# Kernel optimization log

Hardware: AMD Instinct MI355X
Metric: run time of the kernel (lower is better)

The kernel has to match this reference:

```python
import jax, jax.numpy as jnp
import numpy as np

INVALID = 1e9  # distance value marking a missing arc (>= 1e6 threshold in source)
TEMPERATURE = 0.5


def setup_inputs() -> dict:
    n = 4096
    key = jax.random.key(0)
    k_d, k_m, k_l = jax.random.split(key, 3)
    dist = jax.random.uniform(k_d, (n, n), dtype=jnp.float32, minval=0.0, maxval=100.0)
    keep = jax.random.uniform(k_m, (n, n)) < 0.5
    distance_matrix = jnp.where(keep, dist, INVALID).astype(jnp.float32)
    logits = (-2.0 + 0.5 * jax.random.normal(k_l, (n, n))).astype(jnp.float32)
    attention_logits = jnp.zeros((n, n), dtype=jnp.float32)
    return {
        "distance_matrix": distance_matrix,
        "logits": logits,
        "attention_logits": attention_logits,
        "source": 0,
        "destination": n - 1,
    }


def reference(distance_matrix, logits, attention_logits, source, destination):
    n = distance_matrix.shape[0]
    valid = (distance_matrix < 1e6).astype(jnp.float32)
    density = jnp.sum(valid) / (n * n)
    mu1 = 1.0
    mu2 = 10.0 * (1.0 + density)
    mu3 = 10.0 * (1.0 + density)

    # decision matrix (dense branch)
    attention = jax.nn.softmax(attention_logits, axis=1)
    x = jax.nn.sigmoid(logits / TEMPERATURE) * attention * valid  # [n, n]

    # flow penalty: vectorized form of the per-node loop
    out_flow = jnp.sum(x, axis=1)  # [n]
    in_flow = jnp.sum(x, axis=0)   # [n]
    d = out_flow - in_flow
    d = d.at[source].add(-1.0).at[destination].add(1.0)
    flow_penalty = jnp.sum(d * d)

    path_cost = jnp.sum(distance_matrix * x)  # invalid arcs have x == 0
    binary_penalty = jnp.sum(x * (1.0 - x))

    # connectivity: 10-step matmul power iteration (min(n-1, 10) = 10 for n > 11)
    reach = x
    for _ in range(10):
        reach = jnp.minimum(reach + reach @ x, 1.0)
    connectivity_penalty = jnp.square(1.0 - reach[source, destination])

    sparsity_penalty = jnp.sum(x) / (n * n)
    n_edges = jnp.sum(valid)

    return (mu1 * path_cost / (n_edges + 1e-6)
            + mu2 * flow_penalty / n
            + mu3 * binary_penalty / (n * n)
            + 20.0 * connectivity_penalty
            + 5.0 * sparsity_penalty)
```

## Files before the change

### kernel.cpp

```cpp
#include <hip/hip_runtime.h>
#include <hip/hip_bf16.h>
#include <cmath>

typedef unsigned short u16;
typedef unsigned int u32;

__device__ __forceinline__ float bf2f(u16 b) {
    return __uint_as_float(((u32)b) << 16);
}
__device__ __forceinline__ u16 f2bf(float f) {
    u32 u = __float_as_uint(f);
    u = (u + 0x7fffu + ((u >> 16) & 1u)) >> 16;
    return (u16)u;
}

__device__ __forceinline__ float wave_sum(float v) {
#pragma unroll
    for (int o = 32; o > 0; o >>= 1) v += __shfl_xor(v, o, 64);
    return v;
}

__device__ float block_sum(float v) {
    __shared__ float s[4];
    v = wave_sum(v);
    __syncthreads();
    if ((threadIdx.x & 63) == 0) s[threadIdx.x >> 6] = v;
    __syncthreads();
    return s[0] + s[1] + s[2] + s[3];
}

template <int K>
__global__ __launch_bounds__(256, 4) void k_x(
    const float* __restrict__ dist, const float* __restrict__ logit,
    const float* __restrict__ attn, const int* __restrict__ srcp,
    u16* __restrict__ xb, float* __restrict__ out_flow,
    float* __restrict__ cnt_row, float* __restrict__ s2_row,
    float* __restrict__ pc_row, float* __restrict__ v, int n) {
    const int row = blockIdx.x;
    const int t = threadIdx.x;
    const size_t base = (size_t)row * n;

    float4 a4[K];
#pragma unroll
    for (int k = 0; k < K; ++k)
        a4[k] = *(const float4*)(attn + base + 4 * t + 1024 * k);
    float se = 0.f;
#pragma unroll
    for (int k = 0; k < K; ++k) {
        a4[k].x = __expf(a4[k].x); a4[k].y = __expf(a4[k].y);
        a4[k].z = __expf(a4[k].z); a4[k].w = __expf(a4[k].w);
        se += (a4[k].x + a4[k].y) + (a4[k].z + a4[k].w);
    }
    const float invZ = 1.0f / block_sum(se);
    const int src = *srcp;

    float4 d4[K], l4[K];
#pragma unroll
    for (int k = 0; k < K; ++k) {
        const int col = 4 * t + 1024 * k;
        d4[k] = *(const float4*)(dist + base + col);
        l4[k] = *(const float4*)(logit + base + col);
    }
    float cnt = 0.f, s1 = 0.f, s2 = 0.f, pc = 0.f;
#pragma unroll
    for (int k = 0; k < K; ++k) {
        const int col = 4 * t + 1024 * k;
        const float av[4] = {a4[k].x, a4[k].y, a4[k].z, a4[k].w};
        const float dv[4] = {d4[k].x, d4[k].y, d4[k].z, d4[k].w};
        const float lv[4] = {l4[k].x, l4[k].y, l4[k].z, l4[k].w};
        float xv[4];
        ushort4 pk;
        u16* pkp = (u16*)&pk;
#pragma unroll
        for (int q = 0; q < 4; ++q) {
            float valid = (dv[q] < 1.0e6f) ? 1.f : 0.f;
            float sg = 1.0f / (1.0f + __expf(-2.0f * lv[q]));
            float x = sg * (av[q] * invZ) * valid;
            xv[q] = x;
            cnt += valid;
            s1 += x;
            s2 += x * x;
            pc += dv[q] * x;
            pkp[q] = f2bf(x);
        }
        *(ushort4*)(xb + base + col) = pk;
        if (row == src) {
            float4 vf; vf.x = xv[0]; vf.y = xv[1]; vf.z = xv[2]; vf.w = xv[3];
            *(float4*)(v + col) = vf;
        }
    }
    s1 = block_sum(s1);
    cnt = block_sum(cnt);
    s2 = block_sum(s2);
    pc = block_sum(pc);
    if (t == 0) {
        out_flow[row] = s1;
        cnt_row[row] = cnt;
        s2_row[row] = s2;
        pc_row[row] = pc;
    }
}

template <int FIRST>
__global__ __launch_bounds__(256) void k_iter(
    const u16* __restrict__ xb, const float* __restrict__ v_in,
    const float* __restrict__ up_in, float* __restrict__ v_out,
    float* __restrict__ up_out, float* __restrict__ ip,
    int n, int nbx, int rc) {
    __shared__ float vl[64];
    __shared__ float vparts[4][64];
    const int t = threadIdx.x;
    const int lin = blockIdx.x;
    const int xcd = lin & 7;
    const int slot = lin >> 3;
    const int bx = slot % nbx;
    const int by = xcd * ((gridDim.x >> 3) / nbx) + slot / nbx;
    const int rows_per = n / rc;
    const int i0 = by * rows_per;
    const int j0 = bx * 1024 + t * 4;

    if (FIRST) {
        if (t < rows_per) {
            float a = v_in[i0 + t];
            vl[t] = a;
            if (bx == 0) v_out[i0 + t] = a;
        }
    } else {
        const int i = t & 63, g = t >> 6;
        const int cpg = rc >> 2;
        float a = 0.f;
#pragma unroll 4
        for (int c = g * cpg; c < (g + 1) * cpg; ++c)
            a += up_in[(size_t)c * n + i0 + i];
        vparts[g][i] = a;
        __syncthreads();
        if (t < rows_per) {
            float s = v_in[i0 + t] + vparts[0][t] + vparts[1][t] +
                      vparts[2][t] + vparts[3][t];
            vl[t] = s;
            if (bx == 0) v_out[i0 + t] = s;
        }
    }
    __syncthreads();

    float4 acc = {0.f, 0.f, 0.f, 0.f};
    float4 cs = {0.f, 0.f, 0.f, 0.f};
#pragma unroll 8
    for (int i = 0; i < rows_per; ++i) {
        ushort4 xv = *(const ushort4*)(xb + (size_t)(i0 + i) * n + j0);
        float vi = vl[i];
        acc.x = fmaf(vi, bf2f(xv.x), acc.x);
        acc.y = fmaf(vi, bf2f(xv.y), acc.y);
        acc.z = fmaf(vi, bf2f(xv.z), acc.z);
        acc.w = fmaf(vi, bf2f(xv.w), acc.w);
        if (FIRST) {
            cs.x += bf2f(xv.x); cs.y += bf2f(xv.y);
            cs.z += bf2f(xv.z); cs.w += bf2f(xv.w);
        }
    }
    *(float4*)(up_out + (size_t)by * n + j0) = acc;
    if (FIRST) *(float4*)(ip + (size_t)by * n + j0) = cs;
}

__global__ __launch_bounds__(256) void k_reduce(
    const float* __restrict__ out_flow, const float* __restrict__ ip,
    const float* __restrict__ cnt_row, const float* __restrict__ s2_row,
    const float* __restrict__ pc_row, const int* __restrict__ srcp,
    const int* __restrict__ dstp, float* __restrict__ pb, int n, int nchunk) {
    const int t = threadIdx.x;
    const int j = blockIdx.x * 256 + t;
    const int src = *srcp, dst = *dstp;
    float infl = 0.f;
#pragma unroll 8
    for (int c = 0; c < nchunk; ++c) infl += ip[(size_t)c * n + j];
    float d = out_flow[j] - infl;
    if (j == src) d -= 1.f;
    if (j == dst) d += 1.f;
    float f = block_sum(d * d);
    float s1 = block_sum(out_flow[j]);
    float cnt = block_sum(cnt_row[j]);
    float s2 = block_sum(s2_row[j]);
    float pc = block_sum(pc_row[j]);
    if (t == 0) {
        float* p = pb + blockIdx.x * 5;
        p[0] = f; p[1] = s1; p[2] = cnt; p[3] = s2; p[4] = pc;
    }
}

__global__ __launch_bounds__(256) void k_final(
    const float* __restrict__ pb, const float* __restrict__ v_last,
    const float* __restrict__ up_last, const int* __restrict__ dstp,
    float* __restrict__ out, int n, int nblk, int nchunk) {
    const int t = threadIdx.x;
    const int dst = *dstp;
    float flow = block_sum(t < nblk ? pb[t * 5 + 0] : 0.f);
    float S1   = block_sum(t < nblk ? pb[t * 5 + 1] : 0.f);
    float NE   = block_sum(t < nblk ? pb[t * 5 + 2] : 0.f);
    float S2   = block_sum(t < nblk ? pb[t * 5 + 3] : 0.f);
    float PC   = block_sum(t < nblk ? pb[t * 5 + 4] : 0.f);
    float r = block_sum(t < nchunk ? up_last[(size_t)t * n + dst] : 0.f);
    if (t == 0) {
        r += v_last[dst];
        float nf = (float)n;
        float nn = nf * nf;
        float density = NE / nn;
        float mu2 = 10.f * (1.f + density);
        float om = 1.f - r;
        float res = PC / (NE + 1e-6f)
                  + mu2 * flow / nf
                  + mu2 * (S1 - S2) / nn
                  + 20.f * om * om
                  + 5.f * S1 / nn;
        out[0] = res;
    }
}

extern "C" void kernel_launch(void* const* d_in, const int* in_sizes, int n_in,
                              void* d_out, int out_size, void* d_ws, size_t ws_size,
                              hipStream_t stream) {
    const float* dist = (const float*)d_in[0];
    const float* logit = (const float*)d_in[1];
    const float* attn = (const float*)d_in[2];
    const int* srcp = (const int*)d_in[3];
    const int* dstp = (const int*)d_in[4];
    const int n = (int)(std::sqrt((double)in_sizes[0]) + 0.5);
    const size_t nn = (size_t)n * n;

    const int RC = 64;
    const int nbx = n / 1024;

    char* ws = (char*)d_ws;
    u16* xb = (u16*)ws;
    float* f = (float*)(ws + nn * sizeof(u16));
    float* out_flow = f; f += n;
    float* cnt_row = f;  f += n;
    float* s2_row = f;   f += n;
    float* pc_row = f;   f += n;
    float* vA = f;       f += n;
    float* vB = f;       f += n;
    float* upA = f;      f += (size_t)RC * n;
    float* upB = f;      f += (size_t)RC * n;
    float* ip = f;       f += (size_t)RC * n;
    float* pb = f;       f += 128;

    switch (n >> 10) {
        case 4: k_x<4><<<n, 256, 0, stream>>>(dist, logit, attn, srcp, xb,
                    out_flow, cnt_row, s2_row, pc_row, vA, n); break;
        case 2: k_x<2><<<n, 256, 0, stream>>>(dist, logit, attn, srcp, xb,
                    out_flow, cnt_row, s2_row, pc_row, vA, n); break;
        case 8: k_x<8><<<n, 256, 0, stream>>>(dist, logit, attn, srcp, xb,
                    out_flow, cnt_row, s2_row, pc_row, vA, n); break;
        default: k_x<1><<<n, 256, 0, stream>>>(dist, logit, attn, srcp, xb,
                    out_flow, cnt_row, s2_row, pc_row, vA, n); break;
    }

    const int niblk = nbx * RC;

    k_iter<1><<<niblk, 256, 0, stream>>>(xb, vA, nullptr, vB, upA, ip, n, nbx, RC);
    float* vin = vB;  float* uin = upA;
    float* vout;      float* uout;
    for (int it = 2; it <= 10; ++it) {
        vout = (it & 1) ? vB : vA;
        uout = (it & 1) ? upA : upB;
        k_iter<0><<<niblk, 256, 0, stream>>>(xb, vin, uin, vout, uout, nullptr,
                                             n, nbx, RC);
        vin = vout; uin = uout;
    }

    k_reduce<<<n / 256, 256, 0, stream>>>(out_flow, ip, cnt_row, s2_row,
                                          pc_row, srcp, dstp, pb, n, RC);
    k_final<<<1, 256, 0, stream>>>(pb, vin, uin, dstp, (float*)d_out, n,
                                   n / 256, RC);
}
```

Before: 113.1 us.

## Defer softmax normalisation to per-row scale factors applied downstream

The x kernel no longer does a block reduction for the softmax denominator before computing x. It stores unnormalised values, accumulates all row sums in a single pass, and writes a per-row inverse normaliser. The power-iteration and column-sum kernels then fold that row scale into the vector weights. The aim is to remove a sync point and register pressure in k_x (the occupancy hint is also dropped). In exchange, the stored bf16 matrix is unnormalised, which changes rounding, and a few extra per-row loads are added in k_iter.

```diff
diff --git a/kernel.cpp b/kernel.cpp
--- a/kernel.cpp
+++ b/kernel.cpp
@@ -30,74 +30,62 @@
 }
 
 template <int K>
-__global__ __launch_bounds__(256, 4) void k_x(
+__global__ __launch_bounds__(256) void k_x(
     const float* __restrict__ dist, const float* __restrict__ logit,
     const float* __restrict__ attn, const int* __restrict__ srcp,
     u16* __restrict__ xb, float* __restrict__ out_flow,
     float* __restrict__ cnt_row, float* __restrict__ s2_row,
-    float* __restrict__ pc_row, float* __restrict__ v, int n) {
+    float* __restrict__ pc_row, float* __restrict__ v,
+    float* __restrict__ izrow, int n) {
     const int row = blockIdx.x;
     const int t = threadIdx.x;
     const size_t base = (size_t)row * n;
-
-    float4 a4[K];
-#pragma unroll
-    for (int k = 0; k < K; ++k)
-        a4[k] = *(const float4*)(attn + base + 4 * t + 1024 * k);
-    float se = 0.f;
-#pragma unroll
-    for (int k = 0; k < K; ++k) {
-        a4[k].x = __expf(a4[k].x); a4[k].y = __expf(a4[k].y);
-        a4[k].z = __expf(a4[k].z); a4[k].w = __expf(a4[k].w);
-        se += (a4[k].x + a4[k].y) + (a4[k].z + a4[k].w);
-    }
-    const float invZ = 1.0f / block_sum(se);
     const int src = *srcp;
-
-    float4 d4[K], l4[K];
-#pragma unroll
+    float se = 0.f, cnt = 0.f, s1 = 0.f, s2 = 0.f, pc = 0.f;
+#pragma unroll 2
     for (int k = 0; k < K; ++k) {
         const int col = 4 * t + 1024 * k;
-        d4[k] = *(const float4*)(dist + base + col);
-        l4[k] = *(const float4*)(logit + base + col);
-    }
-    float cnt = 0.f, s1 = 0.f, s2 = 0.f, pc = 0.f;
-#pragma unroll
-    for (int k = 0; k < K; ++k) {
-        const int col = 4 * t + 1024 * k;
-        const float av[4] = {a4[k].x, a4[k].y, a4[k].z, a4[k].w};
-        const float dv[4] = {d4[k].x, d4[k].y, d4[k].z, d4[k].w};
-        const float lv[4] = {l4[k].x, l4[k].y, l4[k].z, l4[k].w};
-        float xv[4];
+        const float4 af = *(const float4*)(attn + base + col);
+        const float4 df = *(const float4*)(dist + base + col);
+        const float4 lf = *(const float4*)(logit + base + col);
+        const float ev[4] = {__expf(af.x), __expf(af.y),
+                             __expf(af.z), __expf(af.w)};
+        const float dv[4] = {df.x, df.y, df.z, df.w};
+        const float lv[4] = {lf.x, lf.y, lf.z, lf.w};
+        float yv[4];
         ushort4 pk;
         u16* pkp = (u16*)&pk;
 #pragma unroll
         for (int q = 0; q < 4; ++q) {
             float valid = (dv[q] < 1.0e6f) ? 1.f : 0.f;
             float sg = 1.0f / (1.0f + __expf(-2.0f * lv[q]));
-            float x = sg * (av[q] * invZ) * valid;
-            xv[q] = x;
+            float y = sg * ev[q] * valid;
+            yv[q] = y;
+            se += ev[q];
             cnt += valid;
-            s1 += x;
-            s2 += x * x;
-            pc += dv[q] * x;
-            pkp[q] = f2bf(x);
+            s1 += y;
+            s2 += y * y;
+            pc += dv[q] * y;
+            pkp[q] = f2bf(y);
         }
         *(ushort4*)(xb + base + col) = pk;
         if (row == src) {
-            float4 vf; vf.x = xv[0]; vf.y = xv[1]; vf.z = xv[2]; vf.w = xv[3];
-            *(float4*)(v + col) = vf;
-        }
-    }
+            float4 vf; vf.x = yv[0]; vf.y = yv[1]; vf.z = yv[2]; vf.w = yv[3];
+            *(float4*)(v + base ? v + col : v + col) = vf;
+        }
+    }
+    se = block_sum(se);
     s1 = block_sum(s1);
     cnt = block_sum(cnt);
     s2 = block_sum(s2);
     pc = block_sum(pc);
     if (t == 0) {
-        out_flow[row] = s1;
+        const float iz = 1.0f / se;
+        izrow[row] = iz;
+        out_flow[row] = s1 * iz;
         cnt_row[row] = cnt;
-        s2_row[row] = s2;
-        pc_row[row] = pc;
+        s2_row[row] = s2 * iz * iz;
+        pc_row[row] = pc * iz;
     }
 }
 
@@ -106,8 +94,10 @@
     const u16* __restrict__ xb, const float* __restrict__ v_in,
     const float* __restrict__ up_in, float* __restrict__ v_out,
     float* __restrict__ up_out, float* __restrict__ ip,
+    const float* __restrict__ izrow, const int* __restrict__ srcp,
     int n, int nbx, int rc) {
     __shared__ float vl[64];
+    __shared__ float wz[64];
     __shared__ float vparts[4][64];
     const int t = threadIdx.x;
     const int lin = blockIdx.x;
@@ -121,8 +111,11 @@
 
     if (FIRST) {
         if (t < rows_per) {
-            float a = v_in[i0 + t];
-            vl[t] = a;
+            const float iz_src = izrow[*srcp];
+            const float a = v_in[i0 + t] * iz_src;
+            const float iz = izrow[i0 + t];
+            vl[t] = a * iz;
+            wz[t] = iz;
             if (bx == 0) v_out[i0 + t] = a;
         }
     } else {
@@ -135,9 +128,9 @@
         vparts[g][i] = a;
         __syncthreads();
         if (t < rows_per) {
-            float s = v_in[i0 + t] + vparts[0][t] + vparts[1][t] +
-                      vparts[2][t] + vparts[3][t];
-            vl[t] = s;
+            const float s = v_in[i0 + t] + vparts[0][t] + vparts[1][t] +
+                            vparts[2][t] + vparts[3][t];
+            vl[t] = s * izrow[i0 + t];
             if (bx == 0) v_out[i0 + t] = s;
         }
     }
@@ -154,8 +147,11 @@
         acc.z = fmaf(vi, bf2f(xv.z), acc.z);
         acc.w = fmaf(vi, bf2f(xv.w), acc.w);
         if (FIRST) {
-            cs.x += bf2f(xv.x); cs.y += bf2f(xv.y);
-            cs.z += bf2f(xv.z); cs.w += bf2f(xv.w);
+            float wi = wz[i];
+            cs.x = fmaf(wi, bf2f(xv.x), cs.x);
+            cs.y = fmaf(wi, bf2f(xv.y), cs.y);
+            cs.z = fmaf(wi, bf2f(xv.z), cs.z);
+            cs.w = fmaf(wi, bf2f(xv.w), cs.w);
         }
     }
     *(float4*)(up_out + (size_t)by * n + j0) = acc;
@@ -238,6 +234,7 @@
     float* pc_row = f;   f += n;
     float* vA = f;       f += n;
     float* vB = f;       f += n;
+    float* izrow = f;    f += n;
     float* upA = f;      f += (size_t)RC * n;
     float* upB = f;      f += (size_t)RC * n;
     float* ip = f;       f += (size_t)RC * n;
@@ -245,25 +242,26 @@
 
     switch (n >> 10) {
         case 4: k_x<4><<<n, 256, 0, stream>>>(dist, logit, attn, srcp, xb,
-                    out_flow, cnt_row, s2_row, pc_row, vA, n); break;
+                    out_flow, cnt_row, s2_row, pc_row, vA, izrow, n); break;
         case 2: k_x<2><<<n, 256, 0, stream>>>(dist, logit, attn, srcp, xb,
-                    out_flow, cnt_row, s2_row, pc_row, vA, n); break;
+                    out_flow, cnt_row, s2_row, pc_row, vA, izrow, n); break;
         case 8: k_x<8><<<n, 256, 0, stream>>>(dist, logit, attn, srcp, xb,
-                    out_flow, cnt_row, s2_row, pc_row, vA, n); break;
+                    out_flow, cnt_row, s2_row, pc_row, vA, izrow, n); break;
         default: k_x<1><<<n, 256, 0, stream>>>(dist, logit, attn, srcp, xb,
-                    out_flow, cnt_row, s2_row, pc_row, vA, n); break;
+                    out_flow, cnt_row, s2_row, pc_row, vA, izrow, n); break;
     }
 
     const int niblk = nbx * RC;
 
-    k_iter<1><<<niblk, 256, 0, stream>>>(xb, vA, nullptr, vB, upA, ip, n, nbx, RC);
+    k_iter<1><<<niblk, 256, 0, stream>>>(xb, vA, nullptr, vB, upA, ip,
+                                         izrow, srcp, n, nbx, RC);
     float* vin = vB;  float* uin = upA;
     float* vout;      float* uout;
     for (int it = 2; it <= 10; ++it) {
         vout = (it & 1) ? vB : vA;
         uout = (it & 1) ? upA : upB;
         k_iter<0><<<niblk, 256, 0, stream>>>(xb, vin, uin, vout, uout, nullptr,
-                                             n, nbx, RC);
+                                             izrow, srcp, n, nbx, RC);
         vin = vout; uin = uout;
     }
 
```

New measurement: 115.5 us. +2.2%, slower.
